# Optimization experiments

Measured on AMD Instinct MI355X. Metric: run time of the kernel, lower is better.

## Reference

```python
import jax, jax.numpy as jnp
import numpy as np

N_SRC, N_DST, N_EDGES = 50000, 50000, 500000
IN_DIM, OUT_DIM, EDGE_DIM = 128, 128, 11
BN_EPS = 1e-5


def setup_inputs() -> dict:
    key = jax.random.key(0)
    ks = jax.random.split(key, 16)
    s = 0.05
    return {
        "src_feat": jax.random.normal(ks[0], (N_SRC, IN_DIM), jnp.float32),
        "dst_feat": jax.random.normal(ks[1], (N_DST, IN_DIM), jnp.float32),
        "edge_feats": jax.random.normal(ks[2], (N_EDGES, EDGE_DIM), jnp.float32),
        "src_idx": jax.random.randint(ks[3], (N_EDGES,), 0, N_SRC, jnp.int32),
        "dst_idx": jax.random.randint(ks[4], (N_EDGES,), 0, N_DST, jnp.int32),
        "W_src": jax.random.normal(ks[5], (IN_DIM, OUT_DIM), jnp.float32) * s,
        "b_src": jnp.zeros((OUT_DIM,), jnp.float32),
        "W_dst": jax.random.normal(ks[6], (IN_DIM, OUT_DIM), jnp.float32) * s,
        "b_dst": jnp.zeros((OUT_DIM,), jnp.float32),
        "W_edge": jax.random.normal(ks[7], (EDGE_DIM, OUT_DIM), jnp.float32) * s,
        "b_edge": jnp.zeros((OUT_DIM,), jnp.float32),
        "attn_w": jax.random.normal(ks[8], (3 * OUT_DIM,), jnp.float32) * s,
        "attn_b": jnp.zeros((), jnp.float32),
        "gamma": jnp.ones((OUT_DIM,), jnp.float32),
        "beta": jnp.zeros((OUT_DIM,), jnp.float32),
        "alpha": jnp.asarray(0.25, jnp.float32),
    }


def reference(src_feat, dst_feat, edge_feats, src_idx, dst_idx,
              W_src, b_src, W_dst, b_dst, W_edge, b_edge,
              attn_w, attn_b, gamma, beta, alpha):
    D = W_src.shape[1]
    # project at node/edge level (math identical to projecting gathered feats)
    hs = src_feat @ W_src + b_src            # [Ns, D]  (linear_src)
    hd = dst_feat @ W_dst + b_dst            # [Nd, D]  (linear_dst)
    ep = edge_feats @ W_edge + b_edge        # [E, D]   (linear_edge)
    # attn_l on concat([src, dst, edge]) == sum of three dot products + bias
    aw_s, aw_d, aw_e = attn_w[:D], attn_w[D:2 * D], attn_w[2 * D:]
    a = (hs @ aw_s)[src_idx] + (hd @ aw_d)[dst_idx] + ep @ aw_e + attn_b  # [E]
    # edge softmax over incoming edges of each dst node
    n_dst = dst_feat.shape[0]
    seg_max = jax.ops.segment_max(a, dst_idx, num_segments=n_dst)
    a_exp = jnp.exp(a - seg_max[dst_idx])
    denom = jax.ops.segment_sum(a_exp, dst_idx, num_segments=n_dst)
    attn = a_exp / denom[dst_idx]            # [E]
    # weighted message = attn * linear_src(src_h); scatter-sum to dst
    msg = attn[:, None] * hs[src_idx]        # [E, D]
    h_new = jax.ops.segment_sum(msg, dst_idx, num_segments=n_dst)  # [Nd, D]
    # BatchNorm1d (training-mode batch statistics)
    mean = jnp.mean(h_new, axis=0)
    var = jnp.var(h_new, axis=0)
    h_bn = (h_new - mean) / jnp.sqrt(var + BN_EPS) * gamma + beta
    # PReLU (single shared alpha); dropout is identity in eval
    return jnp.where(h_bn >= 0, h_bn, alpha * h_bn)
```

## Files before the change

### kernel.cpp

```cpp
#include <hip/hip_runtime.h>
#include <cstddef>

#define NSRC 50000
#define NDST 50000
#define NEDGE 500000
#define DIM 128
#define EDIM 11
#define BN_EPS 1e-5f
#define SCAN_NBLK ((NDST + 255) / 256)

#define HS_BLOCKS ((NSRC + 63) / 64)
#define DS_BLOCKS ((NDST + 31) / 32)
#define EDB       ((NEDGE + 511) / 512)
#define SC_BLOCKS ((NEDGE + 1023) / 1024)
#define FUSE_GRID (196 * 9)

typedef short bf16x8 __attribute__((ext_vector_type(8)));
typedef float f32x4 __attribute__((ext_vector_type(4)));

#define OFF_HS       0
#define OFF_SSCORE   (OFF_HS + (size_t)NSRC*DIM/2)
#define OFF_DSCORE   (OFF_SSCORE + NSRC)
#define OFF_EW       (OFF_DSCORE + NDST)
#define OFF_DEG16    (OFF_EW + NEDGE)
#define OFF_COLSUM   (OFF_DEG16 + (size_t)NDST*16)
#define OFF_COLSQ    (OFF_COLSUM + 128)
#define OFF_OFFS     (OFF_COLSQ + 128)
#define OFF_RANK     (OFF_OFFS + NDST + 2)
#define OFF_PAIRS    (OFF_RANK + NEDGE)
#define OFF_WDVEC    (OFF_PAIRS + 2*(size_t)NEDGE)
#define OFF_WEVEC    (OFF_WDVEC + 128)
#define OFF_SCAL     (OFF_WEVEC + 16)
#define OFF_WSVEC    (OFF_SCAL + 4)
#define OFF_PART     (OFF_WSVEC + 128)
#define OFF_WT       (((OFF_PART + 256 + 3) / 4) * 4)

__device__ __forceinline__ unsigned short f2bf(float x) {
    unsigned int u = __float_as_uint(x);
    u += 0x7FFFu + ((u >> 16) & 1u);
    return (unsigned short)(u >> 16);
}
__device__ __forceinline__ float bf2f(unsigned int u16) {
    return __uint_as_float(u16 << 16);
}

__global__ void k_prep(const float* __restrict__ W_dst, const float* __restrict__ b_dst,
                       const float* __restrict__ W_edge, const float* __restrict__ b_edge,
                       const float* __restrict__ W_src, const float* __restrict__ b_src,
                       const float* __restrict__ attn_w, const float* __restrict__ attn_b,
                       float* __restrict__ wd_vec, float* __restrict__ we_vec,
                       float* __restrict__ ws_vec, float* __restrict__ scal) {
    int t = threadIdx.x;
    int bb = blockIdx.x;
    __shared__ float red[128];
    if (bb == 0) {
        float acc = 0.f;
        for (int d = 0; d < DIM; ++d) acc += W_dst[t * DIM + d] * attn_w[DIM + d];
        wd_vec[t] = acc;
        red[t] = b_dst[t] * attn_w[DIM + t];
        __syncthreads();
        for (int s = 64; s > 0; s >>= 1) { if (t < s) red[t] += red[t + s]; __syncthreads(); }
        if (t == 0) scal[0] = red[0];
    } else if (bb == 1) {
        if (t < EDIM) {
            float e = 0.f;
            for (int d = 0; d < DIM; ++d) e += W_edge[t * DIM + d] * attn_w[2 * DIM + d];
            we_vec[t] = e;
        }
        red[t] = b_edge[t] * attn_w[2 * DIM + t];
        __syncthreads();
        for (int s = 64; s > 0; s >>= 1) { if (t < s) red[t] += red[t + s]; __syncthreads(); }
        if (t == 0) scal[1] = red[0] + attn_b[0];
    } else {
        float acc = 0.f;
        for (int d = 0; d < DIM; ++d) acc += W_src[t * DIM + d] * attn_w[d];
        ws_vec[t] = acc;
        red[t] = b_src[t] * attn_w[t];
        __syncthreads();
        for (int s = 64; s > 0; s >>= 1) { if (t < s) red[t] += red[t + s]; __syncthreads(); }
        if (t == 0) scal[2] = red[0];
    }
}

__global__ __launch_bounds__(256) void k_wt(const float* __restrict__ W,
                                            unsigned short* __restrict__ wt) {
    __shared__ float tile[32][33];
    int bi = blockIdx.x & 3;
    int bj = blockIdx.x >> 2;
    int t = threadIdx.x;
    int cl = t & 31;
    #pragma unroll
    for (int i = 0; i < 4; ++i) {
        int kl = (t >> 5) * 4 + i;
        tile[kl][cl] = W[(size_t)(bi * 32 + kl) * DIM + bj * 32 + cl];
    }
    __syncthreads();
    int ko = t & 31;
    #pragma unroll
    for (int i = 0; i < 4; ++i) {
        int co = (t >> 5) * 4 + i;
        wt[(size_t)(bj * 32 + co) * DIM + bi * 32 + ko] = f2bf(tile[ko][co]);
    }
}

__global__ __launch_bounds__(256) void k_score(const float* __restrict__ src_feat,
                                               const float* __restrict__ dst_feat,
                                               const float* __restrict__ ws_vec,
                                               const float* __restrict__ wd_vec,
                                               const float* __restrict__ scal,
                                               float* __restrict__ s_score,
                                               float* __restrict__ d_score) {
    int bid = blockIdx.x;
    const float* X;
    const float* V;
    float* out;
    float c;
    int r0;
    if (bid < DS_BLOCKS) {
        X = src_feat; V = ws_vec; out = s_score; c = scal[2]; r0 = bid * 32;
    } else {
        X = dst_feat; V = wd_vec; out = d_score; c = scal[0]; r0 = (bid - DS_BLOCKS) * 32;
    }
    int t = threadIdx.x;
    int row = r0 + (t >> 3);
    int c0 = (t & 7) * 16;
    if (row >= NDST) return;
    const float4* x = reinterpret_cast<const float4*>(X + (size_t)row * DIM + c0);
    const float4* w = reinterpret_cast<const float4*>(V + c0);
    float p = 0.f;
    #pragma unroll
    for (int i = 0; i < 4; ++i) {
        float4 a = x[i], b = w[i];
        p += a.x * b.x + a.y * b.y + a.z * b.z + a.w * b.w;
    }
    p += __shfl_xor(p, 1);
    p += __shfl_xor(p, 2);
    p += __shfl_xor(p, 4);
    if ((t & 7) == 0) out[row] = p + c;
}

__global__ __launch_bounds__(256, 2) void k_fused(const float* __restrict__ A,
                                               const unsigned short* __restrict__ wt,
                                               const float* __restrict__ bias,
                                               const float* __restrict__ ef,
                                               const int* __restrict__ src_idx,
                                               const int* __restrict__ dst_idx,
                                               const float* __restrict__ s_score,
                                               const float* __restrict__ d_score,
                                               const float* __restrict__ we_vec,
                                               const float* __restrict__ scal,
                                               unsigned short* __restrict__ hsb,
                                               float* __restrict__ ew,
                                               int* __restrict__ deg16,
                                               int* __restrict__ rank) {
    const int g = blockIdx.x / 9;
    const int sl = blockIdx.x % 9;
    const int t = threadIdx.x;

    if (sl < 4) {
        const int hb = g * 4 + sl;
        if (hb >= HS_BLOCKS) return;
        const int wv = t >> 6;
        const int lane = t & 63;
        const int lrow = lane & 15;
        const int kg = lane >> 4;
        const int grow = hb * 64 + wv * 16 + lrow;
        const bool rowok = grow < NSRC;
        const float* arow = A + (size_t)grow * DIM;

        bf16x8 af[4];
        #pragma unroll
        for (int s = 0; s < 4; ++s) {
            float4 p0 = make_float4(0.f, 0.f, 0.f, 0.f), p1 = p0;
            if (rowok) {
                p0 = *reinterpret_cast<const float4*>(arow + 32 * s + kg * 8);
                p1 = *reinterpret_cast<const float4*>(arow + 32 * s + kg * 8 + 4);
            }
            bf16x8 a;
            a[0] = (short)f2bf(p0.x); a[1] = (short)f2bf(p0.y);
            a[2] = (short)f2bf(p0.z); a[3] = (short)f2bf(p0.w);
            a[4] = (short)f2bf(p1.x); a[5] = (short)f2bf(p1.y);
            a[6] = (short)f2bf(p1.z); a[7] = (short)f2bf(p1.w);
            af[s] = a;
        }

        f32x4 acc[8];
        #pragma unroll
        for (int c = 0; c < 8; ++c) acc[c] = (f32x4){0.f, 0.f, 0.f, 0.f};

        #pragma unroll
        for (int c = 0; c < 8; ++c) {
            #pragma unroll
            for (int s = 0; s < 4; ++s) {
                const bf16x8 b = *reinterpret_cast<const bf16x8*>(
                    wt + ((size_t)(16 * c + lrow) * DIM + 32 * s + kg * 8));
                acc[c] = __builtin_amdgcn_mfma_f32_16x16x32_bf16(af[s], b, acc[c], 0, 0, 0);
            }
        }

        const int orow0 = hb * 64 + wv * 16 + kg * 4;
        #pragma unroll
        for (int c = 0; c < 8; ++c) {
            float bb = bias[16 * c + lrow];
            #pragma unroll
            for (int i = 0; i < 4; ++i) {
                unsigned int mybf = f2bf(acc[c][i] + bb);
                unsigned int nb = (unsigned int)__shfl_xor((int)mybf, 1);
                int orow = orow0 + i;
                if ((lrow & 1) == 0 && orow < NSRC) {
                    *reinterpret_cast<unsigned int*>(hsb + (size_t)orow * DIM + 16 * c + lrow)
                        = (mybf & 0xFFFFu) | (nb << 16);
                }
            }
        }
    } else {
        const int eb = g * 5 + (sl - 4);
        if (eb >= EDB) return;
        float wvv[EDIM];
        #pragma unroll
        for (int k = 0; k < EDIM; ++k) wvv[k] = we_vec[k];
        const float s1 = scal[1];
        int ebase = eb * 512 + t;
        #pragma unroll
        for (int i = 0; i < 2; ++i) {
            int e = ebase + i * 256;
            if (e < NEDGE) {
                int s = src_idx[e], d = dst_idx[e];
                const float* er = ef + (size_t)e * EDIM;
                float a = s1;
                #pragma unroll
                for (int k = 0; k < EDIM; ++k) a += er[k] * wvv[k];
                a += s_score[s] + d_score[d];
                ew[e] = expf(a);
                rank[e] = atomicAdd(&deg16[(size_t)d * 16], 1);
            }
        }
    }
}

__global__ __launch_bounds__(256) void k_scanA(const int* __restrict__ deg16,
                                               int* __restrict__ off,
                                               int* __restrict__ partials) {
    __shared__ int tmp[256];
    int t = threadIdx.x;
    int i = blockIdx.x * 256 + t;
    int v = (i < NDST) ? deg16[(size_t)i * 16] : 0;
    tmp[t] = v;
    __syncthreads();
    #pragma unroll
    for (int d = 1; d < 256; d <<= 1) {
        int u = (t >= d) ? tmp[t - d] : 0;
        __syncthreads();
        tmp[t] += u;
        __syncthreads();
    }
    if (i < NDST) off[i] = tmp[t] - v;
    if (t == 255) partials[blockIdx.x] = tmp[255];
}

__global__ __launch_bounds__(256) void k_scanB(int* __restrict__ partials) {
    __shared__ int tmp[256];
    int t = threadIdx.x;
    int v = (t < SCAN_NBLK) ? partials[t] : 0;
    tmp[t] = v;
    __syncthreads();
    #pragma unroll
    for (int d = 1; d < 256; d <<= 1) {
        int u = (t >= d) ? tmp[t - d] : 0;
        __syncthreads();
        tmp[t] += u;
        __syncthreads();
    }
    if (t < SCAN_NBLK) partials[t] = tmp[t] - v;
}

__global__ __launch_bounds__(256) void k_scanC(int* __restrict__ off,
                                               const int* __restrict__ partials) {
    int t = threadIdx.x;
    int i = blockIdx.x * 256 + t;
    if (i < NDST) off[i] += partials[blockIdx.x];
    if (i == 0) off[NDST] = NEDGE;
}

__global__ __launch_bounds__(256) void k_scat(const int* __restrict__ src_idx,
                                              const int* __restrict__ dst_idx,
                                              const float* __restrict__ ew,
                                              const int* __restrict__ off,
                                              const int* __restrict__ rank,
                                              int2* __restrict__ pairs) {
    int base = blockIdx.x * 1024 + threadIdx.x;
    #pragma unroll
    for (int i = 0; i < 4; ++i) {
        int e = base + i * 256;
        if (e < NEDGE) {
            int d = dst_idx[e];
            int pos = off[d] + rank[e];
            pairs[pos] = make_int2(src_idx[e], __float_as_int(ew[e]));
        }
    }
}

__global__ __launch_bounds__(256) void k_gather(const unsigned short* __restrict__ hsb,
                                                const int* __restrict__ off,
                                                const int2* __restrict__ pairs,
                                                float* __restrict__ h_new) {
    int wid = (blockIdx.x * blockDim.x + threadIdx.x) >> 6;
    int lane = threadIdx.x & 63;
    if (wid >= NDST) return;
    int b = off[wid], e2 = off[wid + 1];
    int deg = e2 - b;
    const int half = lane >> 5;
    const int c8 = lane & 31;
    float a0 = 0.f, a1 = 0.f, a2 = 0.f, a3 = 0.f, wsum = 0.f;

    for (int base = 0; base < deg; base += 64) {
        int cnt = min(deg - base, 64);
        int myS = 0;
        float myW = 0.f;
        if (lane < cnt) {
            int2 p = pairs[b + base + lane];
            myS = p.x;
            myW = __int_as_float(p.y);
        }
        wsum += myW;

        int j = 0;
        for (; j + 8 <= cnt; j += 8) {
            #pragma unroll
            for (int q = 0; q < 4; ++q) {
                int jj = j + 2 * q + half;
                int s0 = __shfl(myS, jj);
                float w0 = __shfl(myW, jj);
                uint2 v = *reinterpret_cast<const uint2*>(hsb + (size_t)s0 * DIM + c8 * 4);
                a0 += w0 * bf2f(v.x & 0xFFFFu);
                a1 += w0 * bf2f(v.x >> 16);
                a2 += w0 * bf2f(v.y & 0xFFFFu);
                a3 += w0 * bf2f(v.y >> 16);
            }
        }
        for (; j < cnt; j += 2) {
            int jj = j + half;
            int s0 = __shfl(myS, jj);
            float w0 = __shfl(myW, jj);
            uint2 v = *reinterpret_cast<const uint2*>(hsb + (size_t)s0 * DIM + c8 * 4);
            a0 += w0 * bf2f(v.x & 0xFFFFu);
            a1 += w0 * bf2f(v.x >> 16);
            a2 += w0 * bf2f(v.y & 0xFFFFu);
            a3 += w0 * bf2f(v.y >> 16);
        }
    }

    a0 += __shfl_xor(a0, 32);
    a1 += __shfl_xor(a1, 32);
    a2 += __shfl_xor(a2, 32);
    a3 += __shfl_xor(a3, 32);
    #pragma unroll
    for (int m = 1; m < 64; m <<= 1) wsum += __shfl_xor(wsum, m);

    float inv = (deg > 0) ? 1.f / wsum : 0.f;
    if (half == 0) {
        reinterpret_cast<float4*>(h_new + (size_t)wid * DIM)[c8]
            = make_float4(a0 * inv, a1 * inv, a2 * inv, a3 * inv);
    }
}

__global__ __launch_bounds__(256) void k_bnstats(const float* __restrict__ h,
                                                 float* __restrict__ colsum,
                                                 float* __restrict__ colsq) {
    int col = threadIdx.x & 127;
    int rp = threadIdx.x >> 7;
    float s = 0.f, q = 0.f;
    for (int r = blockIdx.x * 2 + rp; r < NDST; r += gridDim.x * 2) {
        float x = h[(size_t)r * DIM + col];
        s += x;
        q += x * x;
    }
    __shared__ float ls[2][128], lq[2][128];
    ls[rp][col] = s;
    lq[rp][col] = q;
    __syncthreads();
    if (rp == 0) {
        atomicAdd(&colsum[col], ls[0][col] + ls[1][col]);
        atomicAdd(&colsq[col], lq[0][col] + lq[1][col]);
    }
}

__global__ __launch_bounds__(256) void k_bnfinal(float* __restrict__ h,
                                                 const float* __restrict__ colsum,
                                                 const float* __restrict__ colsq,
                                                 const float* __restrict__ gamma,
                                                 const float* __restrict__ beta,
                                                 const float* __restrict__ alpha_p) {
    const size_t total4 = (size_t)NDST * DIM / 4;
    const float alpha = alpha_p[0];
    const float invN = 1.f / (float)NDST;
    const int c0 = (threadIdx.x & 31) * 4;
    float sc[4], sh[4];
    #pragma unroll
    for (int k = 0; k < 4; ++k) {
        float mean = colsum[c0 + k] * invN;
        float var = colsq[c0 + k] * invN - mean * mean;
        float s = gamma[c0 + k] * rsqrtf(var + BN_EPS);
        sc[k] = s;
        sh[k] = beta[c0 + k] - mean * s;
    }
    size_t stride = (size_t)gridDim.x * blockDim.x;
    for (size_t i = blockIdx.x * blockDim.x + threadIdx.x; i < total4; i += stride) {
        float4 x = reinterpret_cast<float4*>(h)[i];
        float y0 = x.x * sc[0] + sh[0];
        float y1 = x.y * sc[1] + sh[1];
        float y2 = x.z * sc[2] + sh[2];
        float y3 = x.w * sc[3] + sh[3];
        float4 o;
        o.x = y0 >= 0.f ? y0 : alpha * y0;
        o.y = y1 >= 0.f ? y1 : alpha * y1;
        o.z = y2 >= 0.f ? y2 : alpha * y2;
        o.w = y3 >= 0.f ? y3 : alpha * y3;
        reinterpret_cast<float4*>(h)[i] = o;
    }
}

extern "C" void kernel_launch(void* const* d_in, const int* in_sizes, int n_in,
                              void* d_out, int out_size, void* d_ws, size_t ws_size,
                              hipStream_t stream) {
    const float* src_feat   = (const float*)d_in[0];
    const float* dst_feat   = (const float*)d_in[1];
    const float* edge_feats = (const float*)d_in[2];
    const int*   src_idx    = (const int*)d_in[3];
    const int*   dst_idx    = (const int*)d_in[4];
    const float* W_src      = (const float*)d_in[5];
    const float* b_src      = (const float*)d_in[6];
    const float* W_dst      = (const float*)d_in[7];
    const float* b_dst      = (const float*)d_in[8];
    const float* W_edge     = (const float*)d_in[9];
    const float* b_edge     = (const float*)d_in[10];
    const float* attn_w     = (const float*)d_in[11];
    const float* attn_b     = (const float*)d_in[12];
    const float* gamma      = (const float*)d_in[13];
    const float* beta       = (const float*)d_in[14];
    const float* alpha      = (const float*)d_in[15];

    float* ws      = (float*)d_ws;
    unsigned short* hsb = (unsigned short*)(ws + OFF_HS);
    float* s_score = ws + OFF_SSCORE;
    float* d_score = ws + OFF_DSCORE;
    float* ew      = ws + OFF_EW;
    int*   deg16   = (int*)(ws + OFF_DEG16);
    float* colsum  = ws + OFF_COLSUM;
    float* colsq   = ws + OFF_COLSQ;
    int*   off     = (int*)(ws + OFF_OFFS);
    int*   rank    = (int*)(ws + OFF_RANK);
    int2*  pairs   = (int2*)(ws + OFF_PAIRS);
    float* wd_vec  = ws + OFF_WDVEC;
    float* we_vec  = ws + OFF_WEVEC;
    float* scal    = ws + OFF_SCAL;
    float* ws_vec  = ws + OFF_WSVEC;
    int*   part    = (int*)(ws + OFF_PART);
    unsigned short* wt = (unsigned short*)(ws + OFF_WT);

    float* h_new = (float*)d_out;

    hipMemsetAsync(deg16, 0, ((size_t)NDST * 16 + 256) * sizeof(int), stream);

    k_prep<<<3, 128, 0, stream>>>(W_dst, b_dst, W_edge, b_edge, W_src, b_src,
                                  attn_w, attn_b, wd_vec, we_vec, ws_vec, scal);
    k_wt<<<16, 256, 0, stream>>>(W_src, wt);
    k_score<<<2 * DS_BLOCKS, 256, 0, stream>>>(src_feat, dst_feat, ws_vec, wd_vec,
                                               scal, s_score, d_score);
    k_fused<<<FUSE_GRID, 256, 0, stream>>>(src_feat, wt, b_src, edge_feats,
                                           src_idx, dst_idx, s_score, d_score,
                                           we_vec, scal, hsb, ew, deg16, rank);
    k_scanA<<<SCAN_NBLK, 256, 0, stream>>>(deg16, off, part);
    k_scanB<<<1, 256, 0, stream>>>(part);
    k_scanC<<<SCAN_NBLK, 256, 0, stream>>>(off, part);
    k_scat<<<SC_BLOCKS, 256, 0, stream>>>(src_idx, dst_idx, ew, off, rank, pairs);
    k_gather<<<(NDST * 64 + 255) / 256, 256, 0, stream>>>(hsb, off, pairs, h_new);
    k_bnstats<<<512, 256, 0, stream>>>(h_new, colsum, colsq);
    k_bnfinal<<<1024, 256, 0, stream>>>(h_new, colsum, colsq, gamma, beta, alpha);
}
```

Baseline: 139.5 us.

## Merge prep kernels, drop scan fixup pass, batch edge atomics per thread

Merges the attention-vector prep kernel and the W_src transpose kernel into one launch. Removes the third scan pass: consumers now add the per-block partial to the local offset on the fly. The edge part of the fused kernel now covers 8 edges per thread, issuing all degree atomics before the score computation so more of them are in flight, and the grid is rebalanced to 16 GEMM blocks per 5 edge blocks. This cuts two kernel launches in exchange for an extra indexed load in scatter and gather.

```diff
diff --git a/kernel.cpp b/kernel.cpp
--- a/kernel.cpp
+++ b/kernel.cpp
@@ -11,9 +11,10 @@
 
 #define HS_BLOCKS ((NSRC + 63) / 64)
 #define DS_BLOCKS ((NDST + 31) / 32)
-#define EDB       ((NEDGE + 511) / 512)
+#define EDB8      ((NEDGE + 2047) / 2048)
 #define SC_BLOCKS ((NEDGE + 1023) / 1024)
-#define FUSE_GRID (196 * 9)
+#define FUSE_GROUPS 49
+#define FUSE_GRID (FUSE_GROUPS * 21)
 
 typedef short bf16x8 __attribute__((ext_vector_type(8)));
 typedef float f32x4 __attribute__((ext_vector_type(4)));
@@ -44,62 +45,72 @@
     return __uint_as_float(u16 << 16);
 }
 
-__global__ void k_prep(const float* __restrict__ W_dst, const float* __restrict__ b_dst,
-                       const float* __restrict__ W_edge, const float* __restrict__ b_edge,
-                       const float* __restrict__ W_src, const float* __restrict__ b_src,
-                       const float* __restrict__ attn_w, const float* __restrict__ attn_b,
-                       float* __restrict__ wd_vec, float* __restrict__ we_vec,
-                       float* __restrict__ ws_vec, float* __restrict__ scal) {
+__global__ __launch_bounds__(256) void k_prepwt(const float* __restrict__ W_dst,
+                                                const float* __restrict__ b_dst,
+                                                const float* __restrict__ W_edge,
+                                                const float* __restrict__ b_edge,
+                                                const float* __restrict__ W_src,
+                                                const float* __restrict__ b_src,
+                                                const float* __restrict__ attn_w,
+                                                const float* __restrict__ attn_b,
+                                                float* __restrict__ wd_vec,
+                                                float* __restrict__ we_vec,
+                                                float* __restrict__ ws_vec,
+                                                float* __restrict__ scal,
+                                                unsigned short* __restrict__ wt) {
+    int bb = blockIdx.x;
     int t = threadIdx.x;
-    int bb = blockIdx.x;
     __shared__ float red[128];
+    __shared__ float tile[32][33];
     if (bb == 0) {
-        float acc = 0.f;
-        for (int d = 0; d < DIM; ++d) acc += W_dst[t * DIM + d] * attn_w[DIM + d];
-        wd_vec[t] = acc;
-        red[t] = b_dst[t] * attn_w[DIM + t];
+        if (t < 128) {
+            float acc = 0.f;
+            for (int d = 0; d < DIM; ++d) acc += W_dst[t * DIM + d] * attn_w[DIM + d];
+            wd_vec[t] = acc;
+            red[t] = b_dst[t] * attn_w[DIM + t];
+        }
         __syncthreads();
         for (int s = 64; s > 0; s >>= 1) { if (t < s) red[t] += red[t + s]; __syncthreads(); }
         if (t == 0) scal[0] = red[0];
     } else if (bb == 1) {
-        if (t < EDIM) {
-            float e = 0.f;
-            for (int d = 0; d < DIM; ++d) e += W_edge[t * DIM + d] * attn_w[2 * DIM + d];
-            we_vec[t] = e;
-        }
-        red[t] = b_edge[t] * attn_w[2 * DIM + t];
+        if (t < 128) {
+            if (t < EDIM) {
+                float e = 0.f;
+                for (int d = 0; d < DIM; ++d) e += W_edge[t * DIM + d] * attn_w[2 * DIM + d];
+                we_vec[t] = e;
+            }
+            red[t] = b_edge[t] * attn_w[2 * DIM + t];
+        }
         __syncthreads();
         for (int s = 64; s > 0; s >>= 1) { if (t < s) red[t] += red[t + s]; __syncthreads(); }
         if (t == 0) scal[1] = red[0] + attn_b[0];
-    } else {
-        float acc = 0.f;
-        for (int d = 0; d < DIM; ++d) acc += W_src[t * DIM + d] * attn_w[d];
-        ws_vec[t] = acc;
-        red[t] = b_src[t] * attn_w[t];
+    } else if (bb == 2) {
+        if (t < 128) {
+            float acc = 0.f;
+            for (int d = 0; d < DIM; ++d) acc += W_src[t * DIM + d] * attn_w[d];
+            ws_vec[t] = acc;
+            red[t] = b_src[t] * attn_w[t];
+        }
         __syncthreads();
         for (int s = 64; s > 0; s >>= 1) { if (t < s) red[t] += red[t + s]; __syncthreads(); }
         if (t == 0) scal[2] = red[0];
-    }
-}
-
-__global__ __launch_bounds__(256) void k_wt(const float* __restrict__ W,
-                                            unsigned short* __restrict__ wt) {
-    __shared__ float tile[32][33];
-    int bi = blockIdx.x & 3;
-    int bj = blockIdx.x >> 2;
-    int t = threadIdx.x;
-    int cl = t & 31;
-    #pragma unroll
-    for (int i = 0; i < 4; ++i) {
-        int kl = (t >> 5) * 4 + i;
-        tile[kl][cl] = W[(size_t)(bi * 32 + kl) * DIM + bj * 32 + cl];
-    }
-    __syncthreads();
-    int ko = t & 31;
-    #pragma unroll
-    for (int i = 0; i < 4; ++i) {
-        int co = (t >> 5) * 4 + i;
-        wt[(size_t)(bj * 32 + co) * DIM + bi * 32 + ko] = f2bf(tile[ko][co]);
+    } else {
+        int idx = bb - 3;
+        int bi = idx & 3;
+        int bj = idx >> 2;
+        int cl = t & 31;
+        #pragma unroll
+        for (int i = 0; i < 4; ++i) {
+            int kl = (t >> 5) * 4 + i;
+            tile[kl][cl] = W_src[(size_t)(bi * 32 + kl) * DIM + bj * 32 + cl];
+        }
+        __syncthreads();
+        int ko = t & 31;
+        #pragma unroll
+        for (int i = 0; i < 4; ++i) {
+            int co = (t >> 5) * 4 + i;
+            wt[(size_t)(bj * 32 + co) * DIM + bi * 32 + ko] = f2bf(tile[ko][co]);
+        }
     }
 }
 
@@ -153,12 +164,12 @@
                                                float* __restrict__ ew,
                                                int* __restrict__ deg16,
                                                int* __restrict__ rank) {
-    const int g = blockIdx.x / 9;
-    const int sl = blockIdx.x % 9;
+    const int g = blockIdx.x / 21;
+    const int sl = blockIdx.x % 21;
     const int t = threadIdx.x;
 
-    if (sl < 4) {
-        const int hb = g * 4 + sl;
+    if (sl < 16) {
+        const int hb = g * 16 + sl;
         if (hb >= HS_BLOCKS) return;
         const int wv = t >> 6;
         const int lane = t & 63;
@@ -214,32 +225,50 @@
             }
         }
     } else {
-        const int eb = g * 5 + (sl - 4);
-        if (eb >= EDB) return;
+        const int eb = g * 5 + (sl - 16);
+        if (eb >= EDB8) return;
+        const int ebase = eb * 2048 + t;
+
+        int ds[8];
+        #pragma unroll
+        for (int i = 0; i < 8; ++i) {
+            int e = ebase + i * 256;
+            ds[i] = (e < NEDGE) ? dst_idx[e] : 0;
+        }
+        int rk[8];
+        #pragma unroll
+        for (int i = 0; i < 8; ++i) {
+            int e = ebase + i * 256;
+            if (e < NEDGE) rk[i] = atomicAdd(&deg16[(size_t)ds[i] * 16], 1);
+        }
+        #pragma unroll
+        for (int i = 0; i < 8; ++i) {
+            int e = ebase + i * 256;
+            if (e < NEDGE) rank[e] = rk[i];
+        }
+
         float wvv[EDIM];
         #pragma unroll
         for (int k = 0; k < EDIM; ++k) wvv[k] = we_vec[k];
         const float s1 = scal[1];
-        int ebase = eb * 512 + t;
-        #pragma unroll
-        for (int i = 0; i < 2; ++i) {
+        #pragma unroll
+        for (int i = 0; i < 8; ++i) {
             int e = ebase + i * 256;
             if (e < NEDGE) {
-                int s = src_idx[e], d = dst_idx[e];
+                int s = src_idx[e];
                 const float* er = ef + (size_t)e * EDIM;
                 float a = s1;
                 #pragma unroll
                 for (int k = 0; k < EDIM; ++k) a += er[k] * wvv[k];
-                a += s_score[s] + d_score[d];
+                a += s_score[s] + d_score[ds[i]];
                 ew[e] = expf(a);
-                rank[e] = atomicAdd(&deg16[(size_t)d * 16], 1);
             }
         }
     }
 }
 
 __global__ __launch_bounds__(256) void k_scanA(const int* __restrict__ deg16,
-                                               int* __restrict__ off,
+                                               int* __restrict__ offL,
                                                int* __restrict__ partials) {
     __shared__ int tmp[256];
     int t = threadIdx.x;
@@ -254,7 +283,7 @@
         tmp[t] += u;
         __syncthreads();
     }
-    if (i < NDST) off[i] = tmp[t] - v;
+    if (i < NDST) offL[i] = tmp[t] - v;
     if (t == 255) partials[blockIdx.x] = tmp[255];
 }
 
@@ -274,18 +303,11 @@
     if (t < SCAN_NBLK) partials[t] = tmp[t] - v;
 }
 
-__global__ __launch_bounds__(256) void k_scanC(int* __restrict__ off,
-                                               const int* __restrict__ partials) {
-    int t = threadIdx.x;
-    int i = blockIdx.x * 256 + t;
-    if (i < NDST) off[i] += partials[blockIdx.x];
-    if (i == 0) off[NDST] = NEDGE;
-}
-
 __global__ __launch_bounds__(256) void k_scat(const int* __restrict__ src_idx,
                                               const int* __restrict__ dst_idx,
                                               const float* __restrict__ ew,
-                                              const int* __restrict__ off,
+                                              const int* __restrict__ offL,
+                                              const int* __restrict__ part,
                                               const int* __restrict__ rank,
                                               int2* __restrict__ pairs) {
     int base = blockIdx.x * 1024 + threadIdx.x;
@@ -294,20 +316,22 @@
         int e = base + i * 256;
         if (e < NEDGE) {
             int d = dst_idx[e];
-            int pos = off[d] + rank[e];
+            int pos = offL[d] + part[d >> 8] + rank[e];
             pairs[pos] = make_int2(src_idx[e], __float_as_int(ew[e]));
         }
     }
 }
 
 __global__ __launch_bounds__(256) void k_gather(const unsigned short* __restrict__ hsb,
-                                                const int* __restrict__ off,
+                                                const int* __restrict__ offL,
+                                                const int* __restrict__ part,
                                                 const int2* __restrict__ pairs,
                                                 float* __restrict__ h_new) {
     int wid = (blockIdx.x * blockDim.x + threadIdx.x) >> 6;
     int lane = threadIdx.x & 63;
     if (wid >= NDST) return;
-    int b = off[wid], e2 = off[wid + 1];
+    int b = offL[wid] + part[wid >> 8];
+    int e2 = (wid + 1 < NDST) ? (offL[wid + 1] + part[(wid + 1) >> 8]) : NEDGE;
     int deg = e2 - b;
     const int half = lane >> 5;
     const int c8 = lane & 31;
@@ -448,7 +472,7 @@
     int*   deg16   = (int*)(ws + OFF_DEG16);
     float* colsum  = ws + OFF_COLSUM;
     float* colsq   = ws + OFF_COLSQ;
-    int*   off     = (int*)(ws + OFF_OFFS);
+    int*   offL    = (int*)(ws + OFF_OFFS);
     int*   rank    = (int*)(ws + OFF_RANK);
     int2*  pairs   = (int2*)(ws + OFF_PAIRS);
     float* wd_vec  = ws + OFF_WDVEC;
@@ -462,19 +486,17 @@
 
     hipMemsetAsync(deg16, 0, ((size_t)NDST * 16 + 256) * sizeof(int), stream);
 
-    k_prep<<<3, 128, 0, stream>>>(W_dst, b_dst, W_edge, b_edge, W_src, b_src,
-                                  attn_w, attn_b, wd_vec, we_vec, ws_vec, scal);
-    k_wt<<<16, 256, 0, stream>>>(W_src, wt);
+    k_prepwt<<<19, 256, 0, stream>>>(W_dst, b_dst, W_edge, b_edge, W_src, b_src,
+                                     attn_w, attn_b, wd_vec, we_vec, ws_vec, scal, wt);
     k_score<<<2 * DS_BLOCKS, 256, 0, stream>>>(src_feat, dst_feat, ws_vec, wd_vec,
                                                scal, s_score, d_score);
     k_fused<<<FUSE_GRID, 256, 0, stream>>>(src_feat, wt, b_src, edge_feats,
                                            src_idx, dst_idx, s_score, d_score,
                                            we_vec, scal, hsb, ew, deg16, rank);
-    k_scanA<<<SCAN_NBLK, 256, 0, stream>>>(deg16, off, part);
+    k_scanA<<<SCAN_NBLK, 256, 0, stream>>>(deg16, offL, part);
     k_scanB<<<1, 256, 0, stream>>>(part);
-    k_scanC<<<SCAN_NBLK, 256, 0, stream>>>(off, part);
-    k_scat<<<SC_BLOCKS, 256, 0, stream>>>(src_idx, dst_idx, ew, off, rank, pairs);
-    k_gather<<<(NDST * 64 + 255) / 256, 256, 0, stream>>>(hsb, off, pairs, h_new);
+    k_scat<<<SC_BLOCKS, 256, 0, stream>>>(src_idx, dst_idx, ew, offL, part, rank, pairs);
+    k_gather<<<(NDST * 64 + 255) / 256, 256, 0, stream>>>(hsb, offL, part, pairs, h_new);
     k_bnstats<<<512, 256, 0, stream>>>(h_new, colsum, colsq);
     k_bnfinal<<<1024, 256, 0, stream>>>(h_new, colsum, colsq, gamma, beta, alpha);
 }
```

Result: slower. 143.0 us (+2.5%).
